# Kernel optimization log

Hardware: AMD Instinct MI355X
Metric: run time of the kernel (lower is better)

## Reference

```python
import jax, jax.numpy as jnp
import numpy as np

HIDDEN = 768
KV_DIM = HIDDEN // 3  # 256
BATCH, SEQ = 2, 8192
THETA = 10000.0


def rope_table(seq_len, dim):
    # Matches LlamaRotaryEmbedding: returns [1, seq_len, dim] sinusoid table
    pos = jnp.arange(seq_len, dtype=jnp.float32)                       # [S]
    freqs = THETA ** (-jnp.arange(0, dim, 2, dtype=jnp.float32) / dim)  # [dim/2]
    ang = pos[:, None] * freqs[None, :]                                 # [S, dim/2]
    return jnp.concatenate([jnp.sin(ang), jnp.cos(ang)], axis=-1)[None]  # [1, S, dim]


def setup_inputs() -> dict:
    key = jax.random.key(0)
    kx, kq, kk, kv, ko = jax.random.split(key, 5)
    s = 1.0 / np.sqrt(HIDDEN)
    return {
        "x": jax.random.normal(kx, (BATCH, SEQ, HIDDEN), dtype=jnp.float32),
        # torch nn.Linear weights: [out_features, in_features], y = x @ W.T
        "Wq": jax.random.uniform(kq, (HIDDEN, HIDDEN), jnp.float32, -s, s),
        "Wk": jax.random.uniform(kk, (KV_DIM, HIDDEN), jnp.float32, -s, s),
        "Wv": jax.random.uniform(kv, (KV_DIM, HIDDEN), jnp.float32, -s, s),
        "Wo": jax.random.uniform(ko, (HIDDEN, KV_DIM), jnp.float32, -s, s),
    }


def reference(x, Wq, Wk, Wv, Wo):
    B, S, H = x.shape
    # q/k projections are computed in the original but immediately OVERWRITTEN
    # by the rope table (the rope module ignores its input values). Kept here
    # for faithfulness; XLA will DCE them in forward.
    q = jnp.einsum('bsh,oh->bso', x, Wq)
    k = jnp.einsum('bsh,oh->bso', x, Wk)
    v = jnp.einsum('bsh,oh->bso', x, Wv)                # [B, S, KV_DIM]
    r = rope_table(S, H)                                 # [1, S, H] -> q == k == r
    attn_weights = jnp.matmul(r, jnp.swapaxes(r, -2, -1))  # [1, S, S]
    attn_probs = jax.nn.softmax(attn_weights, axis=-1)      # [1, S, S]
    attn_output = jnp.matmul(attn_probs, v)                 # broadcast -> [B, S, KV_DIM]
    out = jnp.einsum('bsk,ok->bso', attn_output, Wo)        # [B, S, H]
    return out
```

## Files before the change

### kernel.cpp

```cpp
#include <hip/hip_runtime.h>


typedef unsigned short u16;
typedef __attribute__((ext_vector_type(8))) short short8;
typedef __attribute__((ext_vector_type(4))) float float4v;

__device__ inline u16 f32_to_bf16(float f) {
  union { float f; unsigned int u; } v; v.f = f;
  unsigned int r = v.u + 0x7FFF + ((v.u >> 16) & 1);
  return (u16)(r >> 16);
}

__global__ __launch_bounds__(256)
void prep_weights(const float* __restrict__ Wv, const float* __restrict__ Wo,
                  u16* __restrict__ wvt, u16* __restrict__ wot) {
  int id = blockIdx.x * 256 + threadIdx.x;
  union { u16 h[4]; uint2 u; } p;
  if (id < 49152) {
    int e = id * 4, n = e / 768, k = e - n * 768;
    float4v v = *(const float4v*)(Wv + (size_t)n * 768 + k);
    p.h[0] = f32_to_bf16(v[0]); p.h[1] = f32_to_bf16(v[1]);
    p.h[2] = f32_to_bf16(v[2]); p.h[3] = f32_to_bf16(v[3]);
    int t = k >> 5, kk = k & 31;
    *(uint2*)(wvt + ((t * 256 + n) * 32 + kk)) = p.u;
  } else {
    int e = (id - 49152) * 4, n = e / 256, k = e - n * 256;
    float4v v = *(const float4v*)(Wo + (size_t)n * 256 + k);
    p.h[0] = f32_to_bf16(v[0]); p.h[1] = f32_to_bf16(v[1]);
    p.h[2] = f32_to_bf16(v[2]); p.h[3] = f32_to_bf16(v[3]);
    int t = k >> 5, kk = k & 31;
    *(uint2*)(wot + ((t * 768 + n) * 32 + kk)) = p.u;
  }
}

template <bool WS>
__global__ __launch_bounds__(512, 1)
void fused_mfma(const float* __restrict__ x,
                const float* __restrict__ Wv, const float* __restrict__ Wo,
                const u16* __restrict__ wvt, const u16* __restrict__ wot,
                float* __restrict__ out) {
  __shared__ __align__(16) u16 As[64 * 32];
  __shared__ __align__(16) u16 Bs[256 * 32];
  __shared__ __align__(16) u16 Vs[64 * 264];

  const int tid = threadIdx.x;
  const int w  = tid >> 6, l = tid & 63;
  const int q  = l >> 4, mr = l & 15;
  const int wm = w & 1, wn = w >> 1;
  const int row0 = blockIdx.x * 64;

  const int xr = tid >> 3, xg = (tid & 7) * 4;
  const int wr = tid >> 1, wh = (tid & 1) * 16;

  float4v acc[2][4];
#pragma unroll
  for (int i = 0; i < 2; ++i)
#pragma unroll
    for (int j = 0; j < 4; ++j) acc[i][j] = (float4v){0.f, 0.f, 0.f, 0.f};

  for (int kt = 0; kt < 24; ++kt) {
    const int k0 = kt * 32;
    {
      float4v v = *(const float4v*)(x + (size_t)(row0 + xr) * 768 + k0 + xg);
      union { u16 h[4]; uint2 u; } p;
      p.h[0] = f32_to_bf16(v[0]); p.h[1] = f32_to_bf16(v[1]);
      p.h[2] = f32_to_bf16(v[2]); p.h[3] = f32_to_bf16(v[3]);
      *(uint2*)(As + xr * 32 + xg) = p.u;
    }
    if (WS) {
      const u16* g = wvt + (size_t)kt * (256 * 32);
#pragma unroll
      for (int p = 0; p < 2; ++p) {
        int c = tid + p * 512;
        *(short8*)(Bs + c * 8) = *(const short8*)(g + c * 8);
      }
    } else {
      const float* g = Wv + (size_t)wr * 768 + k0 + wh;
      union { u16 h[16]; short8 s[2]; } p;
#pragma unroll
      for (int u = 0; u < 4; ++u) {
        float4v v = *(const float4v*)(g + u * 4);
        p.h[u * 4 + 0] = f32_to_bf16(v[0]); p.h[u * 4 + 1] = f32_to_bf16(v[1]);
        p.h[u * 4 + 2] = f32_to_bf16(v[2]); p.h[u * 4 + 3] = f32_to_bf16(v[3]);
      }
      *(short8*)(Bs + wr * 32 + wh) = p.s[0];
      *(short8*)(Bs + wr * 32 + wh + 8) = p.s[1];
    }
    __syncthreads();

    short8 a[2], b[4];
#pragma unroll
    for (int i = 0; i < 2; ++i)
      a[i] = *(const short8*)(As + (wm * 32 + i * 16 + mr) * 32 + q * 8);
#pragma unroll
    for (int j = 0; j < 4; ++j)
      b[j] = *(const short8*)(Bs + (wn * 64 + j * 16 + mr) * 32 + q * 8);
#pragma unroll
    for (int i = 0; i < 2; ++i)
#pragma unroll
      for (int j = 0; j < 4; ++j)
        acc[i][j] = __builtin_amdgcn_mfma_f32_16x16x32_bf16(a[i], b[j], acc[i][j], 0, 0, 0);
    __syncthreads();
  }

#pragma unroll
  for (int i = 0; i < 2; ++i)
#pragma unroll
    for (int j = 0; j < 4; ++j) {
      int row = wm * 32 + i * 16 + q * 4;
      int col = wn * 64 + j * 16 + mr;
#pragma unroll
      for (int r = 0; r < 4; ++r)
        Vs[(row + r) * 264 + col] = f32_to_bf16(acc[i][j][r]);
    }
  __syncthreads();

  for (int c = 0; c < 3; ++c) {
    float4v acc2[2][4];
#pragma unroll
    for (int i = 0; i < 2; ++i)
#pragma unroll
      for (int j = 0; j < 4; ++j) acc2[i][j] = (float4v){0.f, 0.f, 0.f, 0.f};

    for (int kt = 0; kt < 8; ++kt) {
      const int k0 = kt * 32;
      if (WS) {
        const u16* g = wot + ((size_t)kt * 768 + c * 256) * 32;
#pragma unroll
        for (int p = 0; p < 2; ++p) {
          int cc = tid + p * 512;
          *(short8*)(Bs + cc * 8) = *(const short8*)(g + cc * 8);
        }
      } else {
        const float* g = Wo + (size_t)(c * 256 + wr) * 256 + k0 + wh;
        union { u16 h[16]; short8 s[2]; } p;
#pragma unroll
        for (int u = 0; u < 4; ++u) {
          float4v v = *(const float4v*)(g + u * 4);
          p.h[u * 4 + 0] = f32_to_bf16(v[0]); p.h[u * 4 + 1] = f32_to_bf16(v[1]);
          p.h[u * 4 + 2] = f32_to_bf16(v[2]); p.h[u * 4 + 3] = f32_to_bf16(v[3]);
        }
        *(short8*)(Bs + wr * 32 + wh) = p.s[0];
        *(short8*)(Bs + wr * 32 + wh + 8) = p.s[1];
      }
      __syncthreads();

      short8 a[2], b[4];
#pragma unroll
      for (int i = 0; i < 2; ++i)
        a[i] = *(const short8*)(Vs + (wm * 32 + i * 16 + mr) * 264 + k0 + q * 8);
#pragma unroll
      for (int j = 0; j < 4; ++j)
        b[j] = *(const short8*)(Bs + (wn * 64 + j * 16 + mr) * 32 + q * 8);
#pragma unroll
      for (int i = 0; i < 2; ++i)
#pragma unroll
        for (int j = 0; j < 4; ++j)
          acc2[i][j] = __builtin_amdgcn_mfma_f32_16x16x32_bf16(a[i], b[j], acc2[i][j], 0, 0, 0);
      __syncthreads();
    }

#pragma unroll
    for (int i = 0; i < 2; ++i)
#pragma unroll
      for (int j = 0; j < 4; ++j) {
        int row = row0 + wm * 32 + i * 16 + q * 4;
        int col = c * 256 + wn * 64 + j * 16 + mr;
#pragma unroll
        for (int r = 0; r < 4; ++r)
          out[(size_t)(row + r) * 768 + col] = acc2[i][j][r];
      }
  }
}

extern "C" void kernel_launch(void* const* d_in, const int* in_sizes, int n_in,
                              void* d_out, int out_size, void* d_ws, size_t ws_size,
                              hipStream_t stream) {
  (void)in_sizes; (void)n_in; (void)out_size;
  const float* x  = (const float*)d_in[0];
  const float* Wv = (const float*)d_in[3];
  const float* Wo = (const float*)d_in[4];
  float* out = (float*)d_out;

  if (ws_size >= 786432) {
    u16* wvt = (u16*)d_ws;
    u16* wot = wvt + 196608;
    prep_weights<<<dim3(384), dim3(256), 0, stream>>>(Wv, Wo, wvt, wot);
    fused_mfma<true><<<dim3(256), dim3(512), 0, stream>>>(x, Wv, Wo, wvt, wot, out);
  } else {
    fused_mfma<false><<<dim3(256), dim3(512), 0, stream>>>(x, Wv, Wo, nullptr, nullptr, out);
  }
}
```

Before: 135.8 us.

## Precompute Wo·Wv product and replace fused two-GEMM chain with single GEMM

Adds a prep GEMM that multiplies Wo by Wv into a 768x768 bf16 matrix each call, then computes the output as one GEMM of x against that combined matrix using 128x128 tiles and direct global-to-LDS loads for the weight operand. This removes the intermediate V tile, the second dependent GEMM stage and the one-block-per-CU fused kernel. In exchange it does about 1.5x more multiply-adds per row, and it rounds the combined weights to bf16, which changes the numerics slightly.

```diff
diff --git a/kernel.cpp b/kernel.cpp
--- a/kernel.cpp
+++ b/kernel.cpp
@@ -11,44 +11,163 @@
   return (u16)(r >> 16);
 }
 
+__device__ inline void gld_lds16(const void* g, void* l) {
+  __builtin_amdgcn_global_load_lds(
+      (const __attribute__((address_space(1))) void*)g,
+      (__attribute__((address_space(3))) void*)l, 16, 0, 0);
+}
+
 __global__ __launch_bounds__(256)
-void prep_weights(const float* __restrict__ Wv, const float* __restrict__ Wo,
-                  u16* __restrict__ wvt, u16* __restrict__ wot) {
-  int id = blockIdx.x * 256 + threadIdx.x;
-  union { u16 h[4]; uint2 u; } p;
-  if (id < 49152) {
-    int e = id * 4, n = e / 768, k = e - n * 768;
-    float4v v = *(const float4v*)(Wv + (size_t)n * 768 + k);
-    p.h[0] = f32_to_bf16(v[0]); p.h[1] = f32_to_bf16(v[1]);
-    p.h[2] = f32_to_bf16(v[2]); p.h[3] = f32_to_bf16(v[3]);
-    int t = k >> 5, kk = k & 31;
-    *(uint2*)(wvt + ((t * 256 + n) * 32 + kk)) = p.u;
-  } else {
-    int e = (id - 49152) * 4, n = e / 256, k = e - n * 256;
-    float4v v = *(const float4v*)(Wo + (size_t)n * 256 + k);
-    p.h[0] = f32_to_bf16(v[0]); p.h[1] = f32_to_bf16(v[1]);
-    p.h[2] = f32_to_bf16(v[2]); p.h[3] = f32_to_bf16(v[3]);
-    int t = k >> 5, kk = k & 31;
-    *(uint2*)(wot + ((t * 768 + n) * 32 + kk)) = p.u;
-  }
-}
-
-template <bool WS>
+void gemm_prep(const float* __restrict__ Wo, const float* __restrict__ Wv,
+               u16* __restrict__ M) {
+  __shared__ __align__(16) u16 As[128 * 32];
+  __shared__ __align__(16) u16 Bs[128 * 32];
+
+  const int tid = threadIdx.x;
+  const int w = tid >> 6, l = tid & 63;
+  const int q = l >> 4, mr = l & 15;
+  const int wm = w & 1, wn = w >> 1;
+  const int m0 = blockIdx.y * 128, n0 = blockIdx.x * 128;
+
+  const int ar = tid >> 1, ah = (tid & 1) * 16;
+  const int tk = tid >> 3, tc = (tid & 7) * 16;
+
+  float4v acc[4][4];
+#pragma unroll
+  for (int i = 0; i < 4; ++i)
+#pragma unroll
+    for (int j = 0; j < 4; ++j) acc[i][j] = (float4v){0.f, 0.f, 0.f, 0.f};
+
+  for (int k0 = 0; k0 < 256; k0 += 32) {
+    {
+      union { u16 h[16]; short8 s[2]; } p;
+#pragma unroll
+      for (int u = 0; u < 4; ++u) {
+        float4v v = *(const float4v*)(Wo + (size_t)(m0 + ar) * 256 + k0 + ah + u * 4);
+        p.h[u*4+0] = f32_to_bf16(v[0]); p.h[u*4+1] = f32_to_bf16(v[1]);
+        p.h[u*4+2] = f32_to_bf16(v[2]); p.h[u*4+3] = f32_to_bf16(v[3]);
+      }
+      *(short8*)(As + ar * 32 + ah)     = p.s[0];
+      *(short8*)(As + ar * 32 + ah + 8) = p.s[1];
+    }
+    {
+#pragma unroll
+      for (int u = 0; u < 4; ++u) {
+        float4v v = *(const float4v*)(Wv + (size_t)(k0 + tk) * 768 + n0 + tc + u * 4);
+#pragma unroll
+        for (int f = 0; f < 4; ++f)
+          Bs[(tc + u * 4 + f) * 32 + tk] = f32_to_bf16(v[f]);
+      }
+    }
+    __syncthreads();
+
+    short8 a[4], b[4];
+#pragma unroll
+    for (int i = 0; i < 4; ++i)
+      a[i] = *(const short8*)(As + (wm * 64 + i * 16 + mr) * 32 + q * 8);
+#pragma unroll
+    for (int j = 0; j < 4; ++j)
+      b[j] = *(const short8*)(Bs + (wn * 64 + j * 16 + mr) * 32 + q * 8);
+#pragma unroll
+    for (int i = 0; i < 4; ++i)
+#pragma unroll
+      for (int j = 0; j < 4; ++j)
+        acc[i][j] = __builtin_amdgcn_mfma_f32_16x16x32_bf16(a[i], b[j], acc[i][j], 0, 0, 0);
+    __syncthreads();
+  }
+
+#pragma unroll
+  for (int i = 0; i < 4; ++i)
+#pragma unroll
+    for (int j = 0; j < 4; ++j) {
+      int row = m0 + wm * 64 + i * 16 + q * 4;
+      int col = n0 + wn * 64 + j * 16 + mr;
+#pragma unroll
+      for (int r = 0; r < 4; ++r)
+        M[(size_t)(row + r) * 768 + col] = f32_to_bf16(acc[i][j][r]);
+    }
+}
+
+__global__ __launch_bounds__(256)
+void gemm_xM(const float* __restrict__ A, const u16* __restrict__ B,
+             float* __restrict__ C) {
+  __shared__ __align__(16) u16 As[128 * 32];
+  __shared__ __align__(16) u16 Bs[128 * 32];
+
+  const int tid = threadIdx.x;
+  const int w = tid >> 6, l = tid & 63;
+  const int q = l >> 4, mr = l & 15;
+  const int wm = w & 1, wn = w >> 1;
+  const size_t m0 = (size_t)blockIdx.y * 128;
+  const int n0 = blockIdx.x * 128;
+
+  const int ar = tid >> 1, ah = (tid & 1) * 16;
+  const int bn = w * 16 + (l >> 2), bk = (l & 3) * 8;
+
+  const float* Ap = A + (m0 + ar) * 768 + ah;
+  const u16*   Bp = B + (size_t)(n0 + bn) * 768 + bk;
+
+  float4v acc[4][4];
+#pragma unroll
+  for (int i = 0; i < 4; ++i)
+#pragma unroll
+    for (int j = 0; j < 4; ++j) acc[i][j] = (float4v){0.f, 0.f, 0.f, 0.f};
+
+  for (int k0 = 0; k0 < 768; k0 += 32) {
+    gld_lds16(Bp + k0,            Bs + w * 512);
+    gld_lds16(Bp + 64 * 768 + k0, Bs + 2048 + w * 512);
+    {
+      union { u16 h[16]; short8 s[2]; } p;
+#pragma unroll
+      for (int u = 0; u < 4; ++u) {
+        float4v v = *(const float4v*)(Ap + k0 + u * 4);
+        p.h[u*4+0] = f32_to_bf16(v[0]); p.h[u*4+1] = f32_to_bf16(v[1]);
+        p.h[u*4+2] = f32_to_bf16(v[2]); p.h[u*4+3] = f32_to_bf16(v[3]);
+      }
+      *(short8*)(As + ar * 32 + ah)     = p.s[0];
+      *(short8*)(As + ar * 32 + ah + 8) = p.s[1];
+    }
+    __syncthreads();
+
+    short8 a[4], b[4];
+#pragma unroll
+    for (int i = 0; i < 4; ++i)
+      a[i] = *(const short8*)(As + (wm * 64 + i * 16 + mr) * 32 + q * 8);
+#pragma unroll
+    for (int j = 0; j < 4; ++j)
+      b[j] = *(const short8*)(Bs + (wn * 64 + j * 16 + mr) * 32 + q * 8);
+#pragma unroll
+    for (int i = 0; i < 4; ++i)
+#pragma unroll
+      for (int j = 0; j < 4; ++j)
+        acc[i][j] = __builtin_amdgcn_mfma_f32_16x16x32_bf16(a[i], b[j], acc[i][j], 0, 0, 0);
+    __syncthreads();
+  }
+
+#pragma unroll
+  for (int i = 0; i < 4; ++i)
+#pragma unroll
+    for (int j = 0; j < 4; ++j) {
+      size_t row = m0 + wm * 64 + i * 16 + q * 4;
+      int col = n0 + wn * 64 + j * 16 + mr;
+#pragma unroll
+      for (int r = 0; r < 4; ++r)
+        C[(row + r) * 768 + col] = acc[i][j][r];
+    }
+}
+
 __global__ __launch_bounds__(512, 1)
-void fused_mfma(const float* __restrict__ x,
-                const float* __restrict__ Wv, const float* __restrict__ Wo,
-                const u16* __restrict__ wvt, const u16* __restrict__ wot,
-                float* __restrict__ out) {
+void fused_fallback(const float* __restrict__ x, const float* __restrict__ Wv,
+                    const float* __restrict__ Wo, float* __restrict__ out) {
   __shared__ __align__(16) u16 As[64 * 32];
   __shared__ __align__(16) u16 Bs[256 * 32];
   __shared__ __align__(16) u16 Vs[64 * 264];
 
   const int tid = threadIdx.x;
-  const int w  = tid >> 6, l = tid & 63;
-  const int q  = l >> 4, mr = l & 15;
+  const int w = tid >> 6, l = tid & 63;
+  const int q = l >> 4, mr = l & 15;
   const int wm = w & 1, wn = w >> 1;
   const int row0 = blockIdx.x * 64;
-
   const int xr = tid >> 3, xg = (tid & 7) * 4;
   const int wr = tid >> 1, wh = (tid & 1) * 16;
 
@@ -67,27 +186,19 @@
       p.h[2] = f32_to_bf16(v[2]); p.h[3] = f32_to_bf16(v[3]);
       *(uint2*)(As + xr * 32 + xg) = p.u;
     }
-    if (WS) {
-      const u16* g = wvt + (size_t)kt * (256 * 32);
-#pragma unroll
-      for (int p = 0; p < 2; ++p) {
-        int c = tid + p * 512;
-        *(short8*)(Bs + c * 8) = *(const short8*)(g + c * 8);
-      }
-    } else {
+    {
       const float* g = Wv + (size_t)wr * 768 + k0 + wh;
       union { u16 h[16]; short8 s[2]; } p;
 #pragma unroll
       for (int u = 0; u < 4; ++u) {
         float4v v = *(const float4v*)(g + u * 4);
-        p.h[u * 4 + 0] = f32_to_bf16(v[0]); p.h[u * 4 + 1] = f32_to_bf16(v[1]);
-        p.h[u * 4 + 2] = f32_to_bf16(v[2]); p.h[u * 4 + 3] = f32_to_bf16(v[3]);
-      }
-      *(short8*)(Bs + wr * 32 + wh) = p.s[0];
+        p.h[u*4+0] = f32_to_bf16(v[0]); p.h[u*4+1] = f32_to_bf16(v[1]);
+        p.h[u*4+2] = f32_to_bf16(v[2]); p.h[u*4+3] = f32_to_bf16(v[3]);
+      }
+      *(short8*)(Bs + wr * 32 + wh)     = p.s[0];
       *(short8*)(Bs + wr * 32 + wh + 8) = p.s[1];
     }
     __syncthreads();
-
     short8 a[2], b[4];
 #pragma unroll
     for (int i = 0; i < 2; ++i)
@@ -102,7 +213,6 @@
         acc[i][j] = __builtin_amdgcn_mfma_f32_16x16x32_bf16(a[i], b[j], acc[i][j], 0, 0, 0);
     __syncthreads();
   }
-
 #pragma unroll
   for (int i = 0; i < 2; ++i)
 #pragma unroll
@@ -121,30 +231,21 @@
     for (int i = 0; i < 2; ++i)
 #pragma unroll
       for (int j = 0; j < 4; ++j) acc2[i][j] = (float4v){0.f, 0.f, 0.f, 0.f};
-
     for (int kt = 0; kt < 8; ++kt) {
       const int k0 = kt * 32;
-      if (WS) {
-        const u16* g = wot + ((size_t)kt * 768 + c * 256) * 32;
-#pragma unroll
-        for (int p = 0; p < 2; ++p) {
-          int cc = tid + p * 512;
-          *(short8*)(Bs + cc * 8) = *(const short8*)(g + cc * 8);
-        }
-      } else {
+      {
         const float* g = Wo + (size_t)(c * 256 + wr) * 256 + k0 + wh;
         union { u16 h[16]; short8 s[2]; } p;
 #pragma unroll
         for (int u = 0; u < 4; ++u) {
           float4v v = *(const float4v*)(g + u * 4);
-          p.h[u * 4 + 0] = f32_to_bf16(v[0]); p.h[u * 4 + 1] = f32_to_bf16(v[1]);
-          p.h[u * 4 + 2] = f32_to_bf16(v[2]); p.h[u * 4 + 3] = f32_to_bf16(v[3]);
+          p.h[u*4+0] = f32_to_bf16(v[0]); p.h[u*4+1] = f32_to_bf16(v[1]);
+          p.h[u*4+2] = f32_to_bf16(v[2]); p.h[u*4+3] = f32_to_bf16(v[3]);
         }
-        *(short8*)(Bs + wr * 32 + wh) = p.s[0];
+        *(short8*)(Bs + wr * 32 + wh)     = p.s[0];
         *(short8*)(Bs + wr * 32 + wh + 8) = p.s[1];
       }
       __syncthreads();
-
       short8 a[2], b[4];
 #pragma unroll
       for (int i = 0; i < 2; ++i)
@@ -159,7 +260,6 @@
           acc2[i][j] = __builtin_amdgcn_mfma_f32_16x16x32_bf16(a[i], b[j], acc2[i][j], 0, 0, 0);
       __syncthreads();
     }
-
 #pragma unroll
     for (int i = 0; i < 2; ++i)
 #pragma unroll
@@ -182,12 +282,11 @@
   const float* Wo = (const float*)d_in[4];
   float* out = (float*)d_out;
 
-  if (ws_size >= 786432) {
-    u16* wvt = (u16*)d_ws;
-    u16* wot = wvt + 196608;
-    prep_weights<<<dim3(384), dim3(256), 0, stream>>>(Wv, Wo, wvt, wot);
-    fused_mfma<true><<<dim3(256), dim3(512), 0, stream>>>(x, Wv, Wo, wvt, wot, out);
+  if (ws_size >= 768u * 768u * 2u) {
+    u16* M = (u16*)d_ws;
+    gemm_prep<<<dim3(6, 6), 256, 0, stream>>>(Wo, Wv, M);
+    gemm_xM<<<dim3(6, 128), 256, 0, stream>>>(x, M, out);
   } else {
-    fused_mfma<false><<<dim3(256), dim3(512), 0, stream>>>(x, Wv, Wo, nullptr, nullptr, out);
-  }
-}
+    fused_fallback<<<dim3(256), 512, 0, stream>>>(x, Wv, Wo, out);
+  }
+}
```

After: 161.0 us. 18.5% more time.
